# Performance work log

Measured on AMD Instinct MI355X. Metric: run time of the kernel, lower is better.

The kernel has to match this reference:

```python
import jax, jax.numpy as jnp
import numpy as np

NEG_SLOPE = 0.01  # F.leaky_relu default


def gcn_conv(x, src, dst, W, b):
    """PyG GCNConv: add self-loops, symmetric D^-1/2 (A+I) D^-1/2 normalization."""
    N = x.shape[0]
    loops = jnp.arange(N, dtype=src.dtype)
    src_f = jnp.concatenate([src, loops])  # [E+N]
    dst_f = jnp.concatenate([dst, loops])
    # degree counted on target nodes (includes self-loop), >= 1
    deg = jax.ops.segment_sum(jnp.ones_like(dst_f, dtype=x.dtype), dst_f, num_segments=N)
    dis = jax.lax.rsqrt(deg)  # deg >= 1 so finite
    norm = dis[src_f] * dis[dst_f]  # [E+N]
    h = x @ W  # [N, F_out] linear first (PyG order)
    msg = h[src_f] * norm[:, None]
    out = jax.ops.segment_sum(msg, dst_f, num_segments=N)
    return out + b


def setup_inputs() -> dict:
    key = jax.random.key(0)
    ks = jax.random.split(key, 8)
    N, E = 10000, 320000
    F_in, F1, F2 = 512, 256, 128
    x = jax.random.normal(ks[0], (N, F_in), dtype=jnp.float32)
    edge_index = jax.random.randint(ks[1], (2, E), 0, N, dtype=jnp.int32)
    batch = jnp.zeros((N,), dtype=jnp.int32)
    # Glorot-style params
    W1 = jax.random.normal(ks[2], (F_in, F1), dtype=jnp.float32) * (1.0 / np.sqrt(F_in))
    b1 = jnp.zeros((F1,), dtype=jnp.float32)
    W2 = jax.random.normal(ks[3], (F1, F2), dtype=jnp.float32) * (1.0 / np.sqrt(F1))
    b2 = jnp.zeros((F2,), dtype=jnp.float32)
    return {"x": x, "edge_index": edge_index, "batch": batch,
            "W1": W1, "b1": b1, "W2": W2, "b2": b2}


def reference(x, edge_index, batch, W1, b1, W2, b2):
    src, dst = edge_index[0], edge_index[1]
    h = jax.nn.leaky_relu(gcn_conv(x, src, dst, W1, b1), NEG_SLOPE)
    # dropout is eval-mode identity
    h = jax.nn.leaky_relu(gcn_conv(h, src, dst, W2, b2), NEG_SLOPE)
    x1 = jax.nn.sigmoid(h @ h.T)  # [N, N] dense decode
    return (x1, h)
```

## Files before the change

### kernel.cpp

```cpp
#include <hip/hip_runtime.h>
#include <math.h>

#define LEAKY 0.01f

using short8   = __attribute__((ext_vector_type(8))) short;
using f32x4    = __attribute__((ext_vector_type(4))) float;
using ushort4e = __attribute__((ext_vector_type(4))) unsigned short;

__device__ __forceinline__ ushort f2bf(float f) {
  uint u = __float_as_uint(f);
  uint r = (u + 0x7FFFu + ((u >> 16) & 1u)) >> 16;
  return (ushort)r;
}
__device__ __forceinline__ float bf2f(ushort h) {
  uint u = ((uint)h) << 16;
  return __uint_as_float(u);
}


__global__ void k_count_prep(const int* __restrict__ dst, int* __restrict__ cnt, int E,
                             const float* __restrict__ X, ushort* __restrict__ Xb, long xq,
                             const float* __restrict__ W1, ushort* __restrict__ Wt1,
                             int K1, int N1,
                             const float* __restrict__ W2, ushort* __restrict__ Wt2,
                             int K2, int N2) {
  long i = (long)blockIdx.x * blockDim.x + threadIdx.x;
  if (i < E) atomicAdd(&cnt[dst[i]], 1);
  if (i < xq) {
    long b = i * 4;
    float4 v = *reinterpret_cast<const float4*>(&X[b]);
    ushort4e u = {f2bf(v.x), f2bf(v.y), f2bf(v.z), f2bf(v.w)};
    *reinterpret_cast<ushort4e*>(&Xb[b]) = u;
  } else {
    long j = i - xq;
    long t1 = (long)K1 * N1;
    if (j < t1) {
      int k = (int)(j / N1), n = (int)(j % N1);
      Wt1[(long)n * K1 + k] = f2bf(W1[j]);
    } else if (j < t1 + (long)K2 * N2) {
      long jj = j - t1;
      int k = (int)(jj / N2), n = (int)(jj % N2);
      Wt2[(long)n * K2 + k] = f2bf(W2[jj]);
    }
  }
}

__global__ void k_scan(const int* __restrict__ cnt, int* __restrict__ rowstart,
                       int* __restrict__ cursor, float* __restrict__ dinv,
                       int N, int Etot) {
  __shared__ int part[1024];
  const int t = threadIdx.x;
  const int CH = 16;
  int base = t * CH;
  int local[CH];
  int s = 0;
#pragma unroll
  for (int i = 0; i < CH; i++) {
    int v = (base + i < N) ? cnt[base + i] : 0;
    if (base + i < N) dinv[base + i] = rsqrtf((float)v + 1.0f);
    local[i] = s;
    s += v;
  }
  part[t] = s;
  __syncthreads();
  for (int off = 1; off < 1024; off <<= 1) {
    int add = (t >= off) ? part[t - off] : 0;
    __syncthreads();
    part[t] += add;
    __syncthreads();
  }
  int excl = (t == 0) ? 0 : part[t - 1];
#pragma unroll
  for (int i = 0; i < CH; i++) {
    if (base + i < N) {
      int rs = excl + local[i];
      rowstart[base + i] = rs;
      cursor[base + i] = rs;
    }
  }
  if (t == 0) rowstart[N] = Etot;
}

template <int F, int WAVES, bool LAST>
__global__ __launch_bounds__(64 * WAVES) void k_agg(const ushort* __restrict__ hlin,
                                                    const float* __restrict__ dinv,
                                                    const int* __restrict__ rowstart,
                                                    const unsigned long long* __restrict__ epack,
                                                    const float* __restrict__ bias,
                                                    ushort* __restrict__ aggb,
                                                    float* __restrict__ outh, int N) {
  constexpr int FS = F / WAVES;
  const int node = blockIdx.x;
  const int tid = threadIdx.x;
  const int w = tid >> 6;
  const int lane = tid & 63;
  const int f0 = w * FS + lane * 2;
  const float di = dinv[node];

  float acc0, acc1;
  {
    uint v = *reinterpret_cast<const uint*>(&hlin[(long)node * F + f0]);
    float dd = di * di;
    acc0 = bf2f((ushort)(v & 0xffff)) * dd;
    acc1 = bf2f((ushort)(v >> 16)) * dd;
  }
  const int e0 = rowstart[node], e1 = rowstart[node + 1];
  int e = e0;
  for (; e + 7 < e1; e += 8) {
#pragma unroll
    for (int u = 0; u < 8; u++) {
      unsigned long long pk = epack[e + u];
      int s = (int)(unsigned)(pk & 0xffffffffull);
      float nm = __uint_as_float((uint)(pk >> 32));
      uint v = *reinterpret_cast<const uint*>(&hlin[(long)s * F + f0]);
      acc0 += bf2f((ushort)(v & 0xffff)) * nm;
      acc1 += bf2f((ushort)(v >> 16)) * nm;
    }
  }
  for (; e < e1; e++) {
    unsigned long long pk = epack[e];
    int s = (int)(unsigned)(pk & 0xffffffffull);
    float nm = __uint_as_float((uint)(pk >> 32));
    uint v = *reinterpret_cast<const uint*>(&hlin[(long)s * F + f0]);
    acc0 += bf2f((ushort)(v & 0xffff)) * nm;
    acc1 += bf2f((ushort)(v >> 16)) * nm;
  }

  float v0 = acc0 + bias[f0];
  float v1 = acc1 + bias[f0 + 1];
  v0 = (v0 > 0.f) ? v0 : (LEAKY * v0);
  v1 = (v1 > 0.f) ? v1 : (LEAKY * v1);
  uint o = (uint)f2bf(v0) | ((uint)f2bf(v1) << 16);
  *reinterpret_cast<uint*>(&aggb[(long)node * F + f0]) = o;
  if constexpr (LAST) {
    float2 fo = make_float2(v0, v1);
    *reinterpret_cast<float2*>(&outh[(long)node * F + f0]) = fo;
  }
}

__global__ __launch_bounds__(256) void k_gemm1_csr(
    const ushort* __restrict__ Ab, const ushort* __restrict__ Bb,
    ushort* __restrict__ Cb, int M, int Nc, int K, int ldc, int gemmRows,
    const int* __restrict__ src, const int* __restrict__ dst,
    const float* __restrict__ dinv, int* __restrict__ cursor,
    unsigned long long* __restrict__ epack, int E) {
  constexpr int BM = 64;
  constexpr int MI = BM / 32;
  __shared__ __align__(16) ushort lds[(BM + 128) * 128];

  if (blockIdx.y >= gemmRows) {
    int i = ((blockIdx.y - gemmRows) * 2 + blockIdx.x) * 256 + threadIdx.x;
    if (i < E) {
      int d = dst[i];
      int s = src[i];
      int pos = atomicAdd(&cursor[d], 1);
      float nm = dinv[s] * dinv[d];
      unsigned long long pk = ((unsigned long long)__float_as_uint(nm) << 32) |
                              (unsigned long long)(unsigned)s;
      epack[pos] = pk;
    }
    return;
  }

  ushort* ldsA = lds;
  ushort* ldsB = lds + BM * 128;

  const int tid = threadIdx.x;
  const int lane = tid & 63;
  const int wv = tid >> 6;
  const int wr = wv >> 1, wc = wv & 1;
  const long bm = (long)blockIdx.y * BM;
  const long bn = (long)blockIdx.x * 128;

  f32x4 acc[MI][4];
#pragma unroll
  for (int i = 0; i < MI; i++)
#pragma unroll
    for (int j = 0; j < 4; j++) acc[i][j] = (f32x4){0.f, 0.f, 0.f, 0.f};

  const int kb = ((lane >> 4) << 4);

  for (int k0 = 0; k0 < K; k0 += 128) {
#pragma unroll
    for (int it = 0; it < BM / 16; it++) {
      int off = it * 4096 + tid * 16;
      int row = off >> 8;
      int cb = off & 255;
      long gr = bm + row;
      uint4 v = make_uint4(0u, 0u, 0u, 0u);
      if (gr < M) v = *reinterpret_cast<const uint4*>(&Ab[gr * K + k0 + (cb >> 1)]);
      int sb = (row << 8) | (cb ^ ((row & 7) << 4));
      *reinterpret_cast<uint4*>((char*)ldsA + sb) = v;
    }
#pragma unroll
    for (int it = 0; it < 8; it++) {
      int off = it * 4096 + tid * 16;
      int row = off >> 8;
      int cb = off & 255;
      long gn = bn + row;
      uint4 v = make_uint4(0u, 0u, 0u, 0u);
      if (gn < Nc) v = *reinterpret_cast<const uint4*>(&Bb[gn * K + k0 + (cb >> 1)]);
      int sb = (row << 8) | (cb ^ ((row & 7) << 4));
      *reinterpret_cast<uint4*>((char*)ldsB + sb) = v;
    }
    __syncthreads();

#pragma unroll
    for (int ks = 0; ks < 4; ks++) {
      short8 af[MI], bfr[4];
#pragma unroll
      for (int mi = 0; mi < MI; mi++) {
        int row = wr * (BM / 2) + mi * 16 + (lane & 15);
        int b = ks * 64 + kb;
        int addr = (row << 8) | (b ^ ((row & 7) << 4));
        af[mi] = *reinterpret_cast<const short8*>((const char*)ldsA + addr);
      }
#pragma unroll
      for (int ni = 0; ni < 4; ni++) {
        int row = wc * 64 + ni * 16 + (lane & 15);
        int b = ks * 64 + kb;
        int addr = (row << 8) | (b ^ ((row & 7) << 4));
        bfr[ni] = *reinterpret_cast<const short8*>((const char*)ldsB + addr);
      }
#pragma unroll
      for (int mi = 0; mi < MI; mi++)
#pragma unroll
        for (int ni = 0; ni < 4; ni++)
          acc[mi][ni] = __builtin_amdgcn_mfma_f32_16x16x32_bf16(af[mi], bfr[ni], acc[mi][ni], 0, 0, 0);
    }
    __syncthreads();
  }

#pragma unroll
  for (int ni = 0; ni < 4; ni++) {
    long col = bn + wc * 64 + ni * 16 + (lane & 15);
    if (col >= Nc) continue;
#pragma unroll
    for (int mi = 0; mi < MI; mi++) {
      long rbase2 = bm + wr * (BM / 2) + mi * 16 + ((lane >> 4) << 2);
#pragma unroll
      for (int j = 0; j < 4; j++) {
        long row = rbase2 + j;
        if (row >= M) continue;
        Cb[row * ldc + col] = f2bf(acc[mi][ni][j]);
      }
    }
  }
}

template <int BM>
__global__ __launch_bounds__(256) void k_gemm_bt(const ushort* __restrict__ Ab,
                                                 const ushort* __restrict__ Bb,
                                                 ushort* __restrict__ Cb,
                                                 int M, int N, int K, int ldc) {
  constexpr int MI = BM / 32;
  __shared__ __align__(16) ushort lds[(BM + 128) * 128];
  ushort* ldsA = lds;
  ushort* ldsB = lds + BM * 128;

  const int tid = threadIdx.x;
  const int lane = tid & 63;
  const int wv = tid >> 6;
  const int wr = wv >> 1, wc = wv & 1;
  const long bm = (long)blockIdx.y * BM;
  const long bn = (long)blockIdx.x * 128;

  f32x4 acc[MI][4];
#pragma unroll
  for (int i = 0; i < MI; i++)
#pragma unroll
    for (int j = 0; j < 4; j++) acc[i][j] = (f32x4){0.f, 0.f, 0.f, 0.f};

  const int kb = ((lane >> 4) << 4);

  for (int k0 = 0; k0 < K; k0 += 128) {
#pragma unroll
    for (int it = 0; it < BM / 16; it++) {
      int off = it * 4096 + tid * 16;
      int row = off >> 8;
      int cb = off & 255;
      long gr = bm + row;
      uint4 v = make_uint4(0u, 0u, 0u, 0u);
      if (gr < M) v = *reinterpret_cast<const uint4*>(&Ab[gr * K + k0 + (cb >> 1)]);
      int sb = (row << 8) | (cb ^ ((row & 7) << 4));
      *reinterpret_cast<uint4*>((char*)ldsA + sb) = v;
    }
#pragma unroll
    for (int it = 0; it < 8; it++) {
      int off = it * 4096 + tid * 16;
      int row = off >> 8;
      int cb = off & 255;
      long gn = bn + row;
      uint4 v = make_uint4(0u, 0u, 0u, 0u);
      if (gn < N) v = *reinterpret_cast<const uint4*>(&Bb[gn * K + k0 + (cb >> 1)]);
      int sb = (row << 8) | (cb ^ ((row & 7) << 4));
      *reinterpret_cast<uint4*>((char*)ldsB + sb) = v;
    }
    __syncthreads();

#pragma unroll
    for (int ks = 0; ks < 4; ks++) {
      short8 af[MI], bfr[4];
#pragma unroll
      for (int mi = 0; mi < MI; mi++) {
        int row = wr * (BM / 2) + mi * 16 + (lane & 15);
        int b = ks * 64 + kb;
        int addr = (row << 8) | (b ^ ((row & 7) << 4));
        af[mi] = *reinterpret_cast<const short8*>((const char*)ldsA + addr);
      }
#pragma unroll
      for (int ni = 0; ni < 4; ni++) {
        int row = wc * 64 + ni * 16 + (lane & 15);
        int b = ks * 64 + kb;
        int addr = (row << 8) | (b ^ ((row & 7) << 4));
        bfr[ni] = *reinterpret_cast<const short8*>((const char*)ldsB + addr);
      }
#pragma unroll
      for (int mi = 0; mi < MI; mi++)
#pragma unroll
        for (int ni = 0; ni < 4; ni++)
          acc[mi][ni] = __builtin_amdgcn_mfma_f32_16x16x32_bf16(af[mi], bfr[ni], acc[mi][ni], 0, 0, 0);
    }
    __syncthreads();
  }

#pragma unroll
  for (int ni = 0; ni < 4; ni++) {
    long col = bn + wc * 64 + ni * 16 + (lane & 15);
    if (col >= N) continue;
#pragma unroll
    for (int mi = 0; mi < MI; mi++) {
      long rbase2 = bm + wr * (BM / 2) + mi * 16 + ((lane >> 4) << 2);
#pragma unroll
      for (int j = 0; j < 4; j++) {
        long row = rbase2 + j;
        if (row >= M) continue;
        Cb[row * ldc + col] = f2bf(acc[mi][ni][j]);
      }
    }
  }
}

__global__ __launch_bounds__(256) void k_decode_sym(const ushort* __restrict__ Hb,
                                                    float* __restrict__ C, int N) {
  __shared__ __align__(16) ushort lds[2 * 128 * 128];
  ushort* ldsA = lds;
  ushort* ldsB = lds + 128 * 128;

  const int tid = threadIdx.x;
  const int lane = tid & 63;
  const int wv = tid >> 6;
  const int wr = wv >> 1, wc = wv & 1;

  int t = blockIdx.x;
  int bi = (int)((sqrtf(8.f * (float)t + 1.f) - 1.f) * 0.5f);
  while ((bi + 1) * (bi + 2) / 2 <= t) bi++;
  while (bi * (bi + 1) / 2 > t) bi--;
  int bj = t - bi * (bi + 1) / 2;
  const long bm = (long)bi * 128;
  const long bn = (long)bj * 128;

#pragma unroll
  for (int s = 0; s < 2; s++) {
    long rbase = s ? bn : bm;
    ushort* L = s ? ldsB : ldsA;
#pragma unroll
    for (int it = 0; it < 8; it++) {
      int off = it * 4096 + tid * 16;
      int row = off >> 8;
      int cb = off & 255;
      long grow = rbase + row;
      uint4 v = make_uint4(0u, 0u, 0u, 0u);
      if (grow < N)
        v = *reinterpret_cast<const uint4*>(&Hb[grow * 128 + (cb >> 1)]);
      int sb = (row << 8) | (cb ^ ((row & 7) << 4));
      *reinterpret_cast<uint4*>((char*)L + sb) = v;
    }
  }
  __syncthreads();

  f32x4 acc[4][4];
#pragma unroll
  for (int i = 0; i < 4; i++)
#pragma unroll
    for (int j = 0; j < 4; j++) acc[i][j] = (f32x4){0.f, 0.f, 0.f, 0.f};

  const int kb = ((lane >> 4) << 4);
#pragma unroll
  for (int ks = 0; ks < 4; ks++) {
    short8 af[4], bfr[4];
#pragma unroll
    for (int mi = 0; mi < 4; mi++) {
      int row = wr * 64 + mi * 16 + (lane & 15);
      int b = ks * 64 + kb;
      int addr = (row << 8) | (b ^ ((row & 7) << 4));
      af[mi] = *reinterpret_cast<const short8*>((const char*)ldsA + addr);
    }
#pragma unroll
    for (int ni = 0; ni < 4; ni++) {
      int row = wc * 64 + ni * 16 + (lane & 15);
      int b = ks * 64 + kb;
      int addr = (row << 8) | (b ^ ((row & 7) << 4));
      bfr[ni] = *reinterpret_cast<const short8*>((const char*)ldsB + addr);
    }
#pragma unroll
    for (int mi = 0; mi < 4; mi++)
#pragma unroll
      for (int ni = 0; ni < 4; ni++)
        acc[mi][ni] = __builtin_amdgcn_mfma_f32_16x16x32_bf16(af[mi], bfr[ni], acc[mi][ni], 0, 0, 0);
  }

#pragma unroll
  for (int mi = 0; mi < 4; mi++)
#pragma unroll
    for (int ni = 0; ni < 4; ni++)
#pragma unroll
      for (int j = 0; j < 4; j++)
        acc[mi][ni][j] = __builtin_amdgcn_rcpf(1.f + __expf(-acc[mi][ni][j]));

  if (bi != bj) {
#pragma unroll
    for (int ni = 0; ni < 4; ni++) {
      long gr = bn + wc * 64 + ni * 16 + (lane & 15);
#pragma unroll
      for (int mi = 0; mi < 4; mi++) {
        long gc = bm + wr * 64 + mi * 16 + ((lane >> 4) << 2);
        if (gr < N && gc < N)
          __builtin_nontemporal_store(acc[mi][ni],
                                      reinterpret_cast<f32x4*>(&C[gr * N + gc]));
      }
    }
  }

  __syncthreads();

  float* ft = (float*)lds;
#pragma unroll
  for (int ni = 0; ni < 4; ni++) {
    int col = wc * 64 + ni * 16 + (lane & 15);
#pragma unroll
    for (int mi = 0; mi < 4; mi++) {
      int rb = wr * 64 + mi * 16 + ((lane >> 4) << 2);
#pragma unroll
      for (int j = 0; j < 4; j++) {
        int row = rb + j;
        int byte = (row << 9) + (col << 2);
        byte ^= ((row & 7) << 4);
        *reinterpret_cast<float*>((char*)ft + byte) = acc[mi][ni][j];
      }
    }
  }
  __syncthreads();

#pragma unroll
  for (int it = 0; it < 16; it++) {
    int r = (tid >> 5) + it * 8;
    int ch = tid & 31;
    int byte = (r << 9) + (ch << 4);
    byte ^= ((r & 7) << 4);
    f32x4 v = *reinterpret_cast<const f32x4*>((const char*)ft + byte);
    long gr = bm + r;
    long gc = bn + ch * 4;
    if (gr < N && gc < N)
      __builtin_nontemporal_store(v, reinterpret_cast<f32x4*>(&C[gr * N + gc]));
  }
}


extern "C" void kernel_launch(void* const* d_in, const int* in_sizes, int n_in,
                              void* d_out, int out_size, void* d_ws, size_t ws_size,
                              hipStream_t stream) {
  const float* x  = (const float*)d_in[0];
  const int*   ei = (const int*)d_in[1];
  const float* W1 = (const float*)d_in[3];
  const float* b1 = (const float*)d_in[4];
  const float* W2 = (const float*)d_in[5];
  const float* b2 = (const float*)d_in[6];

  const int N   = in_sizes[2];
  const int E   = in_sizes[1] / 2;
  const int Fin = in_sizes[0] / N;
  const int F1  = in_sizes[4];
  const int F2  = in_sizes[6];

  const int* src = ei;
  const int* dst = ei + E;

  float* ws = (float*)d_ws;
  ushort* w1t      = (ushort*)ws;
  ushort* w2t      = (ushort*)(ws + 65536);
  ushort* xb       = (ushort*)(ws + 81920);
  ushort* h1b      = (ushort*)(ws + 2641920);
  ushort* agg1b    = (ushort*)(ws + 3921920);
  ushort* h2b      = (ushort*)(ws + 5201920);
  ushort* hb       = (ushort*)(ws + 5841920);
  float*  dinv     = ws + 6481920;
  int*    cnt      = (int*)(ws + 6492160);
  int*    cursor   = (int*)(ws + 6502400);
  int*    rowstart = (int*)(ws + 6512640);
  unsigned long long* epack = (unsigned long long*)(ws + 6523136);

  float* out_x1 = (float*)d_out;
  float* out_h  = out_x1 + (long)N * N;

  hipMemsetAsync(cnt, 0, (size_t)N * sizeof(int), stream);
  {
    long xq = (long)N * Fin / 4;
    long tot = xq + (long)Fin * F1 + (long)F1 * F2;
    long thr = (tot > (long)E) ? tot : (long)E;
    k_count_prep<<<(unsigned)((thr + 255) / 256), 256, 0, stream>>>(
        dst, cnt, E, x, xb, xq, W1, w1t, Fin, F1, W2, w2t, F1, F2);
  }
  k_scan<<<1, 1024, 0, stream>>>(cnt, rowstart, cursor, dinv, N, E);

  {
    int gemmRows = (N + 63) / 64;
    int csrRows  = (E + 511) / 512;
    dim3 grid(F1 / 128, gemmRows + csrRows);
    k_gemm1_csr<<<grid, 256, 0, stream>>>(xb, w1t, h1b, N, F1, Fin, F1, gemmRows,
                                          src, dst, dinv, cursor, epack, E);
  }
  k_agg<256, 2, false><<<N, 128, 0, stream>>>(h1b, dinv, rowstart, epack, b1,
                                              agg1b, nullptr, N);

  {
    dim3 grid(F2 / 128, (N + 63) / 64);
    k_gemm_bt<64><<<grid, 256, 0, stream>>>(agg1b, w2t, h2b, N, F2, F1, F2);
  }
  k_agg<128, 1, true><<<N, 64, 0, stream>>>(h2b, dinv, rowstart, epack, b2,
                                            hb, out_h, N);

  {
    int NB = (N + 127) / 128;
    int nblk = NB * (NB + 1) / 2;
    k_decode_sym<<<nblk, 256, 0, stream>>>(hb, out_x1, N);
  }
}
```

Baseline: 233.4 us.

## Load decode MFMA operands directly from global and halve LDS transpose buffer

```diff
diff --git a/kernel.cpp b/kernel.cpp
--- a/kernel.cpp
+++ b/kernel.cpp
@@ -341,11 +341,9 @@
   }
 }
 
-__global__ __launch_bounds__(256) void k_decode_sym(const ushort* __restrict__ Hb,
-                                                    float* __restrict__ C, int N) {
-  __shared__ __align__(16) ushort lds[2 * 128 * 128];
-  ushort* ldsA = lds;
-  ushort* ldsB = lds + 128 * 128;
+__global__ __launch_bounds__(256, 4) void k_decode_sym(const ushort* __restrict__ Hb,
+                                                       float* __restrict__ C, int N) {
+  __shared__ __align__(16) float ft[64 * 128];
 
   const int tid = threadIdx.x;
   const int lane = tid & 63;
@@ -360,24 +358,19 @@
   const long bm = (long)bi * 128;
   const long bn = (long)bj * 128;
 
-#pragma unroll
-  for (int s = 0; s < 2; s++) {
-    long rbase = s ? bn : bm;
-    ushort* L = s ? ldsB : ldsA;
-#pragma unroll
-    for (int it = 0; it < 8; it++) {
-      int off = it * 4096 + tid * 16;
-      int row = off >> 8;
-      int cb = off & 255;
-      long grow = rbase + row;
-      uint4 v = make_uint4(0u, 0u, 0u, 0u);
-      if (grow < N)
-        v = *reinterpret_cast<const uint4*>(&Hb[grow * 128 + (cb >> 1)]);
-      int sb = (row << 8) | (cb ^ ((row & 7) << 4));
-      *reinterpret_cast<uint4*>((char*)L + sb) = v;
-    }
-  }
-  __syncthreads();
+  const int kb = ((lane >> 4) << 4);
+
+  long arow[4], brow[4];
+#pragma unroll
+  for (int mi = 0; mi < 4; mi++) {
+    long r = bm + wr * 64 + mi * 16 + (lane & 15);
+    arow[mi] = (r < N) ? r : (N - 1);
+  }
+#pragma unroll
+  for (int ni = 0; ni < 4; ni++) {
+    long r = bn + wc * 64 + ni * 16 + (lane & 15);
+    brow[ni] = (r < N) ? r : (N - 1);
+  }
 
   f32x4 acc[4][4];
 #pragma unroll
@@ -385,24 +378,16 @@
 #pragma unroll
     for (int j = 0; j < 4; j++) acc[i][j] = (f32x4){0.f, 0.f, 0.f, 0.f};
 
-  const int kb = ((lane >> 4) << 4);
 #pragma unroll
   for (int ks = 0; ks < 4; ks++) {
+    const int cb = (ks * 64 + kb) >> 1;
     short8 af[4], bfr[4];
 #pragma unroll
-    for (int mi = 0; mi < 4; mi++) {
-      int row = wr * 64 + mi * 16 + (lane & 15);
-      int b = ks * 64 + kb;
-      int addr = (row << 8) | (b ^ ((row & 7) << 4));
-      af[mi] = *reinterpret_cast<const short8*>((const char*)ldsA + addr);
-    }
-#pragma unroll
-    for (int ni = 0; ni < 4; ni++) {
-      int row = wc * 64 + ni * 16 + (lane & 15);
-      int b = ks * 64 + kb;
-      int addr = (row << 8) | (b ^ ((row & 7) << 4));
-      bfr[ni] = *reinterpret_cast<const short8*>((const char*)ldsB + addr);
-    }
+    for (int mi = 0; mi < 4; mi++)
+      af[mi] = *reinterpret_cast<const short8*>(&Hb[arow[mi] * 128 + cb]);
+#pragma unroll
+    for (int ni = 0; ni < 4; ni++)
+      bfr[ni] = *reinterpret_cast<const short8*>(&Hb[brow[ni] * 128 + cb]);
 #pragma unroll
     for (int mi = 0; mi < 4; mi++)
 #pragma unroll
@@ -432,37 +417,39 @@
     }
   }
 
-  __syncthreads();
-
-  float* ft = (float*)lds;
-#pragma unroll
-  for (int ni = 0; ni < 4; ni++) {
-    int col = wc * 64 + ni * 16 + (lane & 15);
-#pragma unroll
-    for (int mi = 0; mi < 4; mi++) {
-      int rb = wr * 64 + mi * 16 + ((lane >> 4) << 2);
-#pragma unroll
-      for (int j = 0; j < 4; j++) {
-        int row = rb + j;
-        int byte = (row << 9) + (col << 2);
-        byte ^= ((row & 7) << 4);
-        *reinterpret_cast<float*>((char*)ft + byte) = acc[mi][ni][j];
-      }
-    }
-  }
-  __syncthreads();
-
-#pragma unroll
-  for (int it = 0; it < 16; it++) {
-    int r = (tid >> 5) + it * 8;
-    int ch = tid & 31;
-    int byte = (r << 9) + (ch << 4);
-    byte ^= ((r & 7) << 4);
-    f32x4 v = *reinterpret_cast<const f32x4*>((const char*)ft + byte);
-    long gr = bm + r;
-    long gc = bn + ch * 4;
-    if (gr < N && gc < N)
-      __builtin_nontemporal_store(v, reinterpret_cast<f32x4*>(&C[gr * N + gc]));
+#pragma unroll
+  for (int pass = 0; pass < 2; pass++) {
+    if (wr == pass) {
+#pragma unroll
+      for (int ni = 0; ni < 4; ni++) {
+        int col = wc * 64 + ni * 16 + (lane & 15);
+#pragma unroll
+        for (int mi = 0; mi < 4; mi++) {
+          int rb = mi * 16 + ((lane >> 4) << 2);
+#pragma unroll
+          for (int j = 0; j < 4; j++) {
+            int row = rb + j;
+            int byte = (row << 9) + (col << 2);
+            byte ^= ((row & 7) << 4);
+            *reinterpret_cast<float*>((char*)ft + byte) = acc[mi][ni][j];
+          }
+        }
+      }
+    }
+    __syncthreads();
+#pragma unroll
+    for (int it = 0; it < 8; it++) {
+      int r = (tid >> 5) + it * 8;
+      int ch = tid & 31;
+      int byte = (r << 9) + (ch << 4);
+      byte ^= ((r & 7) << 4);
+      f32x4 v = *reinterpret_cast<const f32x4*>((const char*)ft + byte);
+      long gr = bm + pass * 64 + r;
+      long gc = bn + ch * 4;
+      if (gr < N && gc < N)
+        __builtin_nontemporal_store(v, reinterpret_cast<f32x4*>(&C[gr * N + gc]));
+    }
+    __syncthreads();
   }
 }
 
```

After: 241.6 us. 3.5% more time.
